# Kernel optimization log

Measured on AMD Instinct MI355X. Metric: run time of the kernel, lower is better.

The kernel has to match this reference:

```python
import jax, jax.numpy as jnp
import numpy as np
from jax import lax

V = 100000       # vocab_size / num_words
E = 300          # embedding_size (== num_units, required by compare stage)
M = 300          # num_units / mem_dim
NC = 3           # num_classes
L = 128          # leaves per tree -> N = 2L-1 nodes
N = 2 * L - 1


def build_tree(num_leaves):
    # balanced binary tree, postorder node numbering (children before parent)
    left, right = [], []
    def rec(lo, hi):
        if hi - lo == 1:
            left.append(-1); right.append(-1)
            return len(left) - 1
        mid = (lo + hi) // 2
        l = rec(lo, mid)
        r = rec(mid, hi)
        left.append(l); right.append(r)
        return len(left) - 1
    rec(0, num_leaves)
    return np.asarray(left, np.int32), np.asarray(right, np.int32)


def setup_inputs() -> dict:
    key = jax.random.key(0)
    ks = jax.random.split(key, 20)
    l1, r1 = build_tree(L)
    l2, r2 = build_tree(L)
    s = 0.1  # param scale (stands in for orthogonal init)
    inp = {
        "sent1": jax.random.randint(ks[0], (N,), 0, V),
        "sent2": jax.random.randint(ks[1], (N,), 0, V),
        "left1": jnp.asarray(l1), "right1": jnp.asarray(r1),
        "left2": jnp.asarray(l2), "right2": jnp.asarray(r2),
        "emb": jax.random.normal(ks[2], (V, E), jnp.float32),
        # composer x-projections, gate order: [cx, ix, fx, ox]
        "Wx_i": jax.random.normal(ks[3], (4, M, E), jnp.float32) * s,
        "bx_i": jnp.zeros((4, M), jnp.float32),
        # composer h-projections, gate order: [u, i, lf, rf, o]
        "Wl_i": jax.random.normal(ks[4], (5, M, M), jnp.float32) * s,
        "Wr_i": jax.random.normal(ks[5], (5, M, M), jnp.float32) * s,
        "Wx_c": jax.random.normal(ks[6], (4, M, M), jnp.float32) * s,
        "bx_c": jnp.zeros((4, M), jnp.float32),
        "Wl_c": jax.random.normal(ks[7], (5, M, M), jnp.float32) * s,
        "Wr_c": jax.random.normal(ks[8], (5, M, M), jnp.float32) * s,
        "Wc": jax.random.normal(ks[9], (M, 4 * M), jnp.float32) * 0.01,
        "bc": jnp.zeros((M,), jnp.float32),
        "Wa1": jax.random.normal(ks[10], (M, 4 * M), jnp.float32) * 0.01,
        "ba1": jnp.zeros((M,), jnp.float32),
        "Wa2": jax.random.normal(ks[11], (NC, M), jnp.float32) * 0.01,
        "ba2": jnp.zeros((NC,), jnp.float32),
    }
    return inp


def tree_lstm(xg, left, right, Wl, Wr):
    # xg: [N, 4, M] precomputed x-gate terms (cx, ix, fx, ox)
    # Wl/Wr: [5, M, M] hidden-state gate weights (u, i, lf, rf, o)
    n, _, m = xg.shape
    zero = jnp.zeros((m,), xg.dtype)

    def step(carry, t):
        C, H = carry
        i, l, r = t
        lc = jnp.where(l >= 0, C[jnp.maximum(l, 0)], zero)
        lh = jnp.where(l >= 0, H[jnp.maximum(l, 0)], zero)
        rc = jnp.where(r >= 0, C[jnp.maximum(r, 0)], zero)
        rh = jnp.where(r >= 0, H[jnp.maximum(r, 0)], zero)
        gl = jnp.einsum('gmd,d->gm', Wl, lh)  # [5, M]
        gr = jnp.einsum('gmd,d->gm', Wr, rh)
        x = xg[i]  # [4, M]
        u  = jnp.tanh(x[0] + gl[0] + gr[0])
        ig = jax.nn.sigmoid(x[1] + gl[1] + gr[1])
        lf = jax.nn.sigmoid(x[2] + gl[2] + gr[2])  # fx shared for both forgets (as in source)
        rf = jax.nn.sigmoid(x[2] + gl[3] + gr[3])
        c = ig * u + lf * lc + rf * rc
        o = jax.nn.sigmoid(x[3] + gl[4] + gr[4])
        h = o * jnp.tanh(c)
        return (C.at[i].set(c), H.at[i].set(h)), None

    init = (jnp.zeros((n, m), xg.dtype), jnp.zeros((n, m), xg.dtype))
    (_, H), _ = lax.scan(step, init, (jnp.arange(n), left, right))
    return H  # [N, M] all node hidden states in postorder


def reference(sent1, sent2, left1, right1, left2, right2, emb,
              Wx_i, bx_i, Wl_i, Wr_i, Wx_c, bx_c, Wl_c, Wr_c,
              Wc, bc, Wa1, ba1, Wa2, ba2):
    pad = emb.shape[0] - 1  # num_words - 1

    def encode(sent, left, right):
        # leaves embed their token; internal nodes embed PAD (PAD=True path)
        tok = jnp.where(left < 0, sent, pad)
        x = emb[tok]                                        # [N, E]
        xg = jnp.einsum('nd,gmd->ngm', x, Wx_i) + bx_i      # [N, 4, M]
        return tree_lstm(xg, left, right, Wl_i, Wr_i)

    s1 = encode(sent1, left1, right1)  # [N1, M]
    s2 = encode(sent2, left2, right2)  # [N2, M]

    raw = s1 @ s2.T                                         # [N1, N2]
    beta = jax.nn.softmax(raw, axis=1) @ s2                 # aligned to s1
    alpha = jax.nn.softmax(raw.T, axis=1) @ s1              # aligned to s2

    def compare(s, a, left, right):
        feat = jnp.concatenate([s, a, s - a, s * a], axis=-1)  # [N, 4M]
        h = jax.nn.relu(feat @ Wc.T + bc)                      # [N, M]
        xg = jnp.einsum('nd,gmd->ngm', h, Wx_c) + bx_c
        return tree_lstm(xg, left, right, Wl_c, Wr_c)

    v1 = compare(s1, beta, left1, right1)
    v2 = compare(s2, alpha, left2, right2)

    agg = jnp.concatenate([v1.mean(0), v1.max(0), v2.mean(0), v2.max(0)])  # [4M]
    hidden = jax.nn.relu(agg @ Wa1.T + ba1)
    logits = hidden @ Wa2.T + ba2
    return logits[None, :]  # [1, num_classes]
```

## Files before the change

### kernel.cpp

```cpp
#include <hip/hip_runtime.h>
#include <math.h>

#define NN 255
#define MM 300
#define TC 510
#define NBLK 300
#define CHUNK 16
#define HTLD 512

__device__ __forceinline__ float sigm(float x) { return 1.0f / (1.0f + expf(-x)); }

__device__ __forceinline__ float aload(const float* p) {
  return __hip_atomic_load(p, __ATOMIC_RELAXED, __HIP_MEMORY_SCOPE_AGENT);
}
__device__ __forceinline__ void astore(float* p, float v) {
  __hip_atomic_store(p, v, __ATOMIC_RELAXED, __HIP_MEMORY_SCOPE_AGENT);
}

__device__ __forceinline__ void leaf_gate(const float* __restrict__ xgp, int m, float& c, float& h) {
  float x0 = xgp[m], x1 = xgp[300 + m], x3 = xgp[900 + m];
  float u  = tanhf(x0);
  float ig = sigm(x1);
  c = ig * u;
  h = sigm(x3) * tanhf(c);
}

__device__ __forceinline__ void gsync(unsigned* flags, unsigned phase) {
  asm volatile("s_waitcnt vmcnt(0)" ::: "memory");
  __syncthreads();
  unsigned* gate = flags + NBLK;
  if (blockIdx.x == 0) {
    if (threadIdx.x < 64) {
      for (;;) {
        unsigned mn = phase;
        for (int i = 1 + (int)threadIdx.x; i < NBLK; i += 64)
          mn = min(mn, __hip_atomic_load(&flags[i], __ATOMIC_RELAXED, __HIP_MEMORY_SCOPE_AGENT));
        if (__all(mn >= phase)) break;
        __builtin_amdgcn_s_sleep(2);
      }
      if (threadIdx.x == 0)
        __hip_atomic_store(gate, phase, __ATOMIC_RELAXED, __HIP_MEMORY_SCOPE_AGENT);
    }
  } else {
    if (threadIdx.x == 0) {
      __hip_atomic_store(&flags[blockIdx.x], phase, __ATOMIC_RELAXED, __HIP_MEMORY_SCOPE_AGENT);
      while (__hip_atomic_load(gate, __ATOMIC_RELAXED, __HIP_MEMORY_SCOPE_AGENT) < phase)
        __builtin_amdgcn_s_sleep(2);
    }
  }
  __syncthreads();
}

__global__ __launch_bounds__(512) void k_setup(const int* __restrict__ l1, const int* __restrict__ r1,
                                               const int* __restrict__ l2, const int* __restrict__ r2,
                                               int4* __restrict__ lists2, int* __restrict__ cnt)
{
  __shared__ int lv[TC];
  __shared__ int cs[16];
  int t = threadIdx.x;
  if (t < TC) lv[t] = 0;
  if (t < 16) cs[t] = 0;
  __syncthreads();
  for (int it = 0; it < 12; ++it) {
    int nv = 0;
    if (t < TC) {
      int tr = t >= NN;
      int i  = t - tr * NN;
      const int* L = tr ? l2 : l1;
      const int* R = tr ? r2 : r1;
      int l = L[i], r = R[i];
      nv = (l < 0) ? 0 : 1 + max(lv[tr * NN + l], lv[tr * NN + r]);
    }
    __syncthreads();
    if (t < TC) lv[t] = nv;
    __syncthreads();
  }
  if (t < TC) {
    int tr = t >= NN;
    int i  = t - tr * NN;
    int v  = min(lv[t], 15);
    int pos = atomicAdd(&cs[v], 1);
    int l = (tr ? l2 : l1)[i], r = (tr ? r2 : r1)[i];
    lists2[v * 256 + pos] = make_int4(tr * NN + i, tr * NN + max(l, 0), tr * NN + max(r, 0), 0);
  }
  __syncthreads();
  if (t < 16) cnt[t] = cs[t];
}

__global__ __launch_bounds__(256, 2) void k_tree(
    const int* __restrict__ l1, const int* __restrict__ l2,
    const float* __restrict__ Wl, const float* __restrict__ Wr,
    const float* __restrict__ xg,
    float* __restrict__ H, float* __restrict__ C, float* __restrict__ HT,
    const int4* __restrict__ lists2, const int* __restrict__ cnt,
    unsigned* __restrict__ bar)
{
  __shared__ float Hs[CHUNK][2][320];
  __shared__ float Cs[CHUNK][4][2];
  __shared__ float Xs[CHUNK][4][4];
  __shared__ int4 nfo[288];
  __shared__ int lvoff[9];

  const int tid  = threadIdx.x;
  const int lane = tid & 63;
  const int team = tid >> 6;
  const int mblk = blockIdx.x % 75;
  const int grp  = blockIdx.x / 75;
  const int m    = mblk * 4 + team;

  float wl[5][5], wr[5][5];
  #pragma unroll
  for (int g = 0; g < 5; ++g) {
    #pragma unroll
    for (int j = 0; j < 5; ++j) {
      int d = j * 64 + lane;
      size_t o = ((size_t)g * 300 + m) * 300 + d;
      wl[g][j] = (d < 300) ? Wl[o] : 0.f;
      wr[g][j] = (d < 300) ? Wr[o] : 0.f;
    }
  }

  if (tid == 0) { int o = 0; for (int lv = 1; lv <= 7; ++lv) { lvoff[lv] = o; o += cnt[lv]; } }
  __syncthreads();
  for (int lv = 1; lv <= 7; ++lv)
    for (int i = tid; i < cnt[lv]; i += 256)
      nfo[lvoff[lv] + i] = lists2[lv * 256 + i];

  for (int e = blockIdx.x * 256 + tid; e < TC * 300; e += 256 * NBLK) {
    int gi = e / 300;
    int mm = e - gi * 300;
    int tr = gi >= NN;
    int node = gi - tr * NN;
    if ((tr ? l2 : l1)[node] < 0) {
      float c, h;
      leaf_gate(xg + (size_t)gi * 1200, mm, c, h);
      astore(&C[(size_t)gi * 300 + mm], c);
      astore(&H[(size_t)gi * 300 + mm], h);
      astore(&HT[(size_t)mm * HTLD + gi], h);
    }
  }
  gsync(bar, 1);

  for (int lv = 1; lv <= 7; ++lv) {
    int nodes = cnt[lv];
    int npg = (nodes + 3) >> 2;
    int n0 = grp * npg;
    int n1 = min(nodes, n0 + npg);
    for (int nb = n0; nb < n1; nb += CHUNK) {
      int nch = min(CHUNK, n1 - nb);
      int base = lvoff[lv] + nb;
      __syncthreads();

      #pragma unroll
      for (int p = 0; p < 2; ++p) {
        int niA = team + p * 8;
        int niB = niA + 4;
        bool vA = niA < nch, vB = niB < nch;
        int4 na = vA ? nfo[base + niA] : make_int4(0, 0, 0, 0);
        int4 nb4 = vB ? nfo[base + niB] : make_int4(0, 0, 0, 0);
        float bA0, bA1, bA2, bA3, bA4, bA5, bA6, bA7, bA8, bA9;
        float bB0, bB1, bB2, bB3, bB4, bB5, bB6, bB7, bB8, bB9;
        #define LD(side_ptr, d, ok) ((ok) ? aload(&H[(size_t)(side_ptr) * 300 + (d)]) : 0.f)
        {
          int d0 = lane, d1 = 64 + lane, d2 = 128 + lane, d3 = 192 + lane, d4 = 256 + lane;
          bool i4 = d4 < 300;
          bA0 = LD(na.y, d0, vA); bA1 = LD(na.y, d1, vA); bA2 = LD(na.y, d2, vA);
          bA3 = LD(na.y, d3, vA); bA4 = LD(na.y, d4, vA && i4);
          bA5 = LD(na.z, d0, vA); bA6 = LD(na.z, d1, vA); bA7 = LD(na.z, d2, vA);
          bA8 = LD(na.z, d3, vA); bA9 = LD(na.z, d4, vA && i4);
          bB0 = LD(nb4.y, d0, vB); bB1 = LD(nb4.y, d1, vB); bB2 = LD(nb4.y, d2, vB);
          bB3 = LD(nb4.y, d3, vB); bB4 = LD(nb4.y, d4, vB && i4);
          bB5 = LD(nb4.z, d0, vB); bB6 = LD(nb4.z, d1, vB); bB7 = LD(nb4.z, d2, vB);
          bB8 = LD(nb4.z, d3, vB); bB9 = LD(nb4.z, d4, vB && i4);
          if (vA) {
            Hs[niA][0][d0] = bA0; Hs[niA][0][d1] = bA1; Hs[niA][0][d2] = bA2;
            Hs[niA][0][d3] = bA3; Hs[niA][0][d4] = bA4;
            Hs[niA][1][d0] = bA5; Hs[niA][1][d1] = bA6; Hs[niA][1][d2] = bA7;
            Hs[niA][1][d3] = bA8; Hs[niA][1][d4] = bA9;
          }
          if (vB) {
            Hs[niB][0][d0] = bB0; Hs[niB][0][d1] = bB1; Hs[niB][0][d2] = bB2;
            Hs[niB][0][d3] = bB3; Hs[niB][0][d4] = bB4;
            Hs[niB][1][d0] = bB5; Hs[niB][1][d1] = bB6; Hs[niB][1][d2] = bB7;
            Hs[niB][1][d3] = bB8; Hs[niB][1][d4] = bB9;
          }
        }
        #undef LD
      }
      if (tid < 128) {
        int ni = tid >> 3, tm = (tid >> 1) & 3, side = tid & 1;
        if (ni < nch) {
          int4 nn = nfo[base + ni];
          int child = side ? nn.z : nn.y;
          Cs[ni][tm][side] = aload(&C[(size_t)child * 300 + mblk * 4 + tm]);
        }
      }
      {
        int ni = tid >> 4, tm = (tid >> 2) & 3, g = tid & 3;
        if (ni < nch) {
          int4 nn = nfo[base + ni];
          Xs[ni][tm][g] = xg[(size_t)nn.x * 1200 + g * 300 + mblk * 4 + tm];
        }
      }
      __syncthreads();

      #pragma unroll 2
      for (int ni = 0; ni < nch; ++ni) {
        float p0 = 0.f, p1 = 0.f, p2 = 0.f, p3 = 0.f, p4 = 0.f;
        #pragma unroll
        for (int j = 0; j < 5; ++j) {
          float hl = Hs[ni][0][j * 64 + lane];
          float hr = Hs[ni][1][j * 64 + lane];
          p0 += wl[0][j] * hl + wr[0][j] * hr;
          p1 += wl[1][j] * hl + wr[1][j] * hr;
          p2 += wl[2][j] * hl + wr[2][j] * hr;
          p3 += wl[3][j] * hl + wr[3][j] * hr;
          p4 += wl[4][j] * hl + wr[4][j] * hr;
        }
        #pragma unroll
        for (int off = 32; off; off >>= 1) {
          p0 += __shfl_xor(p0, off);
          p1 += __shfl_xor(p1, off);
          p2 += __shfl_xor(p2, off);
          p3 += __shfl_xor(p3, off);
          p4 += __shfl_xor(p4, off);
        }
        if (lane == 0) {
          int4 nn = nfo[base + ni];
          int gi = nn.x;
          float lc = Cs[ni][team][0], rc = Cs[ni][team][1];
          float u  = tanhf(Xs[ni][team][0] + p0);
          float ig = sigm (Xs[ni][team][1] + p1);
          float lf = sigm (Xs[ni][team][2] + p2);
          float rf = sigm (Xs[ni][team][2] + p3);
          float o  = sigm (Xs[ni][team][3] + p4);
          float cc = ig * u + lf * lc + rf * rc;
          float hv = o * tanhf(cc);
          astore(&C[(size_t)gi * 300 + m], cc);
          astore(&H[(size_t)gi * 300 + m], hv);
          astore(&HT[(size_t)m * HTLD + gi], hv);
        }
      }
    }
    if (lv < 7) gsync(bar, 1 + lv);
  }
}

__global__ __launch_bounds__(256) void k_xg(const int* __restrict__ sent1, const int* __restrict__ sent2,
                                            const int* __restrict__ l1, const int* __restrict__ l2,
                                            const float* __restrict__ emb, int pad,
                                            const float* __restrict__ W, const float* __restrict__ bias,
                                            const float* __restrict__ hsrc, float* __restrict__ out)
{
  __shared__ float Z[8][300];
  int tx = threadIdx.x, ty = threadIdx.y;
  int t = ty * 64 + tx;
  int colbase = blockIdx.y * 8;
  for (int c = 0; c < 8; ++c) {
    int gcol = colbase + c;
    if (gcol < TC) {
      if (hsrc) {
        for (int k = t; k < 300; k += 256) Z[c][k] = hsrc[(size_t)gcol * 300 + k];
      } else {
        int tr = gcol >= NN;
        int node = gcol - tr * NN;
        const int* L = tr ? l2 : l1;
        const int* S = tr ? sent2 : sent1;
        int tok = (L[node] < 0) ? S[node] : pad;
        const float* e = emb + (size_t)tok * 300;
        for (int k = t; k < 300; k += 256) Z[c][k] = e[k];
      }
    } else {
      for (int k = t; k < 300; k += 256) Z[c][k] = 0.f;
    }
  }
  __syncthreads();
  int r = blockIdx.x * 64 + tx;
  if (r < 1200) {
    float a0 = 0.f, a1 = 0.f;
    const float* wp = W + (size_t)r * 300;
    for (int k = 0; k < 300; k += 4) {
      float4 wv = *(const float4*)(wp + k);
      float4 z0 = *(const float4*)(&Z[ty][k]);
      float4 z1 = *(const float4*)(&Z[ty + 4][k]);
      a0 += wv.x*z0.x + wv.y*z0.y + wv.z*z0.z + wv.w*z0.w;
      a1 += wv.x*z1.x + wv.y*z1.y + wv.z*z1.z + wv.w*z1.w;
    }
    float b = bias[r];
    int g0 = colbase + ty, g1 = colbase + ty + 4;
    if (g0 < TC) out[(size_t)g0 * 1200 + r] = a0 + b;
    if (g1 < TC) out[(size_t)g1 * 1200 + r] = a1 + b;
  }
}

__global__ __launch_bounds__(256) void k_attn(const float* __restrict__ H, const float* __restrict__ HT,
                                              float* __restrict__ ab)
{
  __shared__ float q[300];
  __shared__ float pr[NN];
  __shared__ float red[256];
  int b = blockIdx.x, t = threadIdx.x;
  int dir = b >= NN;
  int i = b - dir * NN;
  const float* Ss = H + (dir ? NN * 300 : 0);
  const float* So = H + (dir ? 0 : NN * 300);
  int oppb = dir ? 0 : NN;
  for (int k = t; k < 300; k += 256) q[k] = Ss[(size_t)i * 300 + k];
  __syncthreads();
  float v = -1e30f;
  if (t < NN) {
    float a = 0.f;
    const float* hp = HT + oppb + t;
    #pragma unroll 4
    for (int k = 0; k < 300; ++k) a += q[k] * hp[(size_t)k * HTLD];
    pr[t] = a;
    v = a;
  }
  red[t] = v;
  __syncthreads();
  for (int s = 128; s > 0; s >>= 1) { if (t < s) red[t] = fmaxf(red[t], red[t + s]); __syncthreads(); }
  float mx = red[0];
  __syncthreads();
  float e = 0.f;
  if (t < NN) { e = expf(pr[t] - mx); pr[t] = e; }
  red[t] = e;
  __syncthreads();
  for (int s = 128; s > 0; s >>= 1) { if (t < s) red[t] += red[t + s]; __syncthreads(); }
  float inv = 1.0f / red[0];
  __syncthreads();
  for (int m = t; m < 300; m += 256) {
    float a = 0.f;
    for (int j = 0; j < NN; ++j) a += pr[j] * So[(size_t)j * 300 + m];
    ab[(size_t)b * 300 + m] = a * inv;
  }
}

__global__ __launch_bounds__(256) void k_hcmp(const float* __restrict__ Henc, const float* __restrict__ ab,
                                              const float* __restrict__ Wc, const float* __restrict__ bc,
                                              float* __restrict__ hc)
{
  __shared__ float Z[8][1200];
  int tx = threadIdx.x, ty = threadIdx.y;
  int t = ty * 64 + tx;
  int colbase = blockIdx.y * 8;
  for (int c = 0; c < 8; ++c) {
    int gcol = colbase + c;
    if (gcol < TC) {
      const float* sp = Henc + (size_t)gcol * 300;
      const float* ap = ab + (size_t)gcol * 300;
      for (int k = t; k < 1200; k += 256) {
        int sel = k >= 900 ? 3 : (k >= 600 ? 2 : (k >= 300 ? 1 : 0));
        int kk = k - sel * 300;
        float s = sp[kk], a = ap[kk];
        Z[c][k] = sel == 0 ? s : sel == 1 ? a : sel == 2 ? (s - a) : (s * a);
      }
    } else {
      for (int k = t; k < 1200; k += 256) Z[c][k] = 0.f;
    }
  }
  __syncthreads();
  int r = blockIdx.x * 64 + tx;
  if (r < 300) {
    float a0 = 0.f, a1 = 0.f;
    const float* wp = Wc + (size_t)r * 1200;
    for (int k = 0; k < 1200; k += 4) {
      float4 wv = *(const float4*)(wp + k);
      float4 z0 = *(const float4*)(&Z[ty][k]);
      float4 z1 = *(const float4*)(&Z[ty + 4][k]);
      a0 += wv.x*z0.x + wv.y*z0.y + wv.z*z0.z + wv.w*z0.w;
      a1 += wv.x*z1.x + wv.y*z1.y + wv.z*z1.z + wv.w*z1.w;
    }
    float b = bc[r];
    int g0 = colbase + ty, g1 = colbase + ty + 4;
    if (g0 < TC) hc[(size_t)g0 * 300 + r] = fmaxf(a0 + b, 0.f);
    if (g1 < TC) hc[(size_t)g1 * 300 + r] = fmaxf(a1 + b, 0.f);
  }
}

__global__ __launch_bounds__(512) void k_head(const float* __restrict__ HTc,
                                              const float* __restrict__ Wa1, const float* __restrict__ ba1,
                                              const float* __restrict__ Wa2, const float* __restrict__ ba2,
                                              float* __restrict__ out)
{
  __shared__ float a_s[1200];
  __shared__ float hid[300];
  int t = threadIdx.x;
  for (int idx = t; idx < 600; idx += 512) {
    int tr = idx >= 300;
    int m = idx - tr * 300;
    const float* p = HTc + (size_t)m * HTLD + tr * NN;
    float s = 0.f, mx = -1e30f;
    for (int n = 0; n < NN; ++n) { float v = p[n]; s += v; mx = fmaxf(mx, v); }
    a_s[tr * 600 + m] = s / 255.0f;
    a_s[tr * 600 + 300 + m] = mx;
  }
  __syncthreads();
  for (int h = t; h < 300; h += 512) {
    float acc = ba1[h];
    const float* wp = Wa1 + (size_t)h * 1200;
    for (int k = 0; k < 1200; k += 4) {
      float4 wv = *(const float4*)(wp + k);
      float4 av = *(const float4*)(&a_s[k]);
      acc += wv.x*av.x + wv.y*av.y + wv.z*av.z + wv.w*av.w;
    }
    hid[h] = fmaxf(acc, 0.f);
  }
  __syncthreads();
  if (t < 192) {
    int c = t >> 6, lane = t & 63;
    float a = 0.f;
    for (int k = lane; k < 300; k += 64) a += Wa2[c * 300 + k] * hid[k];
    for (int off = 32; off > 0; off >>= 1) a += __shfl_down(a, off);
    if (lane == 0) out[c] = a + ba2[c];
  }
}

extern "C" void kernel_launch(void* const* d_in, const int* in_sizes, int n_in,
                              void* d_out, int out_size, void* d_ws, size_t ws_size,
                              hipStream_t stream)
{
  const int*   sent1 = (const int*)d_in[0];
  const int*   sent2 = (const int*)d_in[1];
  const int*   l1    = (const int*)d_in[2];
  const int*   r1    = (const int*)d_in[3];
  const int*   l2    = (const int*)d_in[4];
  const int*   r2    = (const int*)d_in[5];
  const float* emb   = (const float*)d_in[6];
  const float* Wx_i  = (const float*)d_in[7];
  const float* bx_i  = (const float*)d_in[8];
  const float* Wl_i  = (const float*)d_in[9];
  const float* Wr_i  = (const float*)d_in[10];
  const float* Wx_c  = (const float*)d_in[11];
  const float* bx_c  = (const float*)d_in[12];
  const float* Wl_c  = (const float*)d_in[13];
  const float* Wr_c  = (const float*)d_in[14];
  const float* Wc    = (const float*)d_in[15];
  const float* bc    = (const float*)d_in[16];
  const float* Wa1   = (const float*)d_in[17];
  const float* ba1   = (const float*)d_in[18];
  const float* Wa2   = (const float*)d_in[19];
  const float* ba2   = (const float*)d_in[20];
  int V = in_sizes[6] / 300;
  int pad = V - 1;

  char* w = (char*)d_ws;
  unsigned* bar1 = (unsigned*)w;
  unsigned* bar2 = (unsigned*)(w + 2048);
  int* cnt     = (int*)(w + 4096);
  int4* lists2 = (int4*)(w + 4160);
  float* xg   = (float*)(w + 4160 + 65536);
  float* Henc = xg + 612000;
  float* Hcmp = Henc + 153000;
  float* C    = Hcmp + 153000;
  float* ab   = C + 153000;
  float* hc   = ab + 153000;
  float* HTe  = hc + 153000;
  float* HTc  = HTe + 153600;

  hipMemsetAsync((void*)bar1, 0, 4096, stream);
  k_setup<<<1, 512, 0, stream>>>(l1, r1, l2, r2, lists2, cnt);

  dim3 blk(64, 4);

  k_xg<<<dim3(19, 64), blk, 0, stream>>>(sent1, sent2, l1, l2, emb, pad, Wx_i, bx_i, nullptr, xg);
  {
    void* args[] = {(void*)&l1, (void*)&l2,
                    (void*)&Wl_i, (void*)&Wr_i, (void*)&xg,
                    (void*)&Henc, (void*)&C, (void*)&HTe,
                    (void*)&lists2, (void*)&cnt, (void*)&bar1};
    hipLaunchCooperativeKernel((void*)k_tree, dim3(NBLK), dim3(256), args, 0, stream);
  }

  k_attn<<<TC, 256, 0, stream>>>(Henc, HTe, ab);

  k_hcmp<<<dim3(5, 64), blk, 0, stream>>>(Henc, ab, Wc, bc, hc);
  k_xg<<<dim3(19, 64), blk, 0, stream>>>(sent1, sent2, l1, l2, emb, pad, Wx_c, bx_c, hc, xg);
  {
    void* args[] = {(void*)&l1, (void*)&l2,
                    (void*)&Wl_c, (void*)&Wr_c, (void*)&xg,
                    (void*)&Hcmp, (void*)&C, (void*)&HTc,
                    (void*)&lists2, (void*)&cnt, (void*)&bar2};
    hipLaunchCooperativeKernel((void*)k_tree, dim3(NBLK), dim3(256), args, 0, stream);
  }

  k_head<<<1, 512, 0, stream>>>(HTc, Wa1, ba1, Wa2, ba2, (float*)d_out);
}
```

Baseline: 503.8 us.

## Fuse whole pipeline into one persistent cooperative kernel with grid barriers

Merges setup, x-projections, both tree-LSTM stages, attention, compare MLP, aggregation and head into a single cooperative kernel of 600 blocks, separated by software grid barriers. The goal is to remove the multiple kernel launches and the gaps between them. Tree levels are now split across 8 node groups instead of 4, with smaller chunks and packed 32-bit child lists. The cost is many more grid-wide barriers with 600 participating blocks, and a fallback to the old multi-kernel path when the occupancy check fails.

```diff
diff --git a/kernel.cpp b/kernel.cpp
--- a/kernel.cpp
+++ b/kernel.cpp
@@ -2,54 +2,433 @@
 #include <math.h>
 
 #define NN 255
-#define MM 300
 #define TC 510
-#define NBLK 300
-#define CHUNK 16
 #define HTLD 512
-
-__device__ __forceinline__ float sigm(float x) { return 1.0f / (1.0f + expf(-x)); }
-
-__device__ __forceinline__ float aload(const float* p) {
-  return __hip_atomic_load(p, __ATOMIC_RELAXED, __HIP_MEMORY_SCOPE_AGENT);
-}
-__device__ __forceinline__ void astore(float* p, float v) {
-  __hip_atomic_store(p, v, __ATOMIC_RELAXED, __HIP_MEMORY_SCOPE_AGENT);
-}
-
-__device__ __forceinline__ void leaf_gate(const float* __restrict__ xgp, int m, float& c, float& h) {
-  float x0 = xgp[m], x1 = xgp[300 + m], x3 = xgp[900 + m];
-  float u  = tanhf(x0);
-  float ig = sigm(x1);
+#define FNB 600
+#define FNG 8
+#define FCH 12
+#define BNB 300
+#define BCH 16
+
+typedef unsigned int uint32;
+
+__device__ __forceinline__ float sigm(float x){ return 1.f/(1.f+expf(-x)); }
+
+__device__ __forceinline__ float aload(const float* p){ return __hip_atomic_load(p, __ATOMIC_RELAXED, __HIP_MEMORY_SCOPE_AGENT); }
+__device__ __forceinline__ void astore(float* p, float v){ __hip_atomic_store(p, v, __ATOMIC_RELAXED, __HIP_MEMORY_SCOPE_AGENT); }
+__device__ __forceinline__ uint32 aloadu(const uint32* p){ return __hip_atomic_load(p, __ATOMIC_RELAXED, __HIP_MEMORY_SCOPE_AGENT); }
+__device__ __forceinline__ void astoreu(uint32* p, uint32 v){ __hip_atomic_store(p, v, __ATOMIC_RELAXED, __HIP_MEMORY_SCOPE_AGENT); }
+
+__device__ __forceinline__ void leaf_gate(const float* __restrict__ xgp, int m, float& c, float& h){
+  float x0 = xgp[m], x1 = xgp[300+m], x3 = xgp[900+m];
+  float u = tanhf(x0), ig = sigm(x1);
   c = ig * u;
   h = sigm(x3) * tanhf(c);
 }
 
-__device__ __forceinline__ void gsync(unsigned* flags, unsigned phase) {
+template<int NB>
+__device__ __forceinline__ void gsync(uint32* flags, uint32 phase){
   asm volatile("s_waitcnt vmcnt(0)" ::: "memory");
   __syncthreads();
-  unsigned* gate = flags + NBLK;
-  if (blockIdx.x == 0) {
-    if (threadIdx.x < 64) {
-      for (;;) {
-        unsigned mn = phase;
-        for (int i = 1 + (int)threadIdx.x; i < NBLK; i += 64)
-          mn = min(mn, __hip_atomic_load(&flags[i], __ATOMIC_RELAXED, __HIP_MEMORY_SCOPE_AGENT));
+  uint32* gate = flags + NB;
+  if (blockIdx.x == 0){
+    if (threadIdx.x < 64){
+      for(;;){
+        uint32 mn = phase;
+        for (int i = 1 + (int)threadIdx.x; i < NB; i += 64)
+          mn = min(mn, aloadu(&flags[i]));
         if (__all(mn >= phase)) break;
         __builtin_amdgcn_s_sleep(2);
       }
-      if (threadIdx.x == 0)
-        __hip_atomic_store(gate, phase, __ATOMIC_RELAXED, __HIP_MEMORY_SCOPE_AGENT);
+      if (threadIdx.x == 0) astoreu(gate, phase);
     }
   } else {
-    if (threadIdx.x == 0) {
-      __hip_atomic_store(&flags[blockIdx.x], phase, __ATOMIC_RELAXED, __HIP_MEMORY_SCOPE_AGENT);
-      while (__hip_atomic_load(gate, __ATOMIC_RELAXED, __HIP_MEMORY_SCOPE_AGENT) < phase)
-        __builtin_amdgcn_s_sleep(2);
-    }
-  }
-  __syncthreads();
-}
+    if (threadIdx.x == 0){
+      astoreu(&flags[blockIdx.x], phase);
+      while (aloadu(gate) < phase) __builtin_amdgcn_s_sleep(2);
+    }
+  }
+  __syncthreads();
+}
+
+__global__ __launch_bounds__(256, 4) void k_all(
+  const int* __restrict__ sent1, const int* __restrict__ sent2,
+  const int* __restrict__ l1, const int* __restrict__ r1,
+  const int* __restrict__ l2, const int* __restrict__ r2,
+  const float* __restrict__ emb, int pad,
+  const float* __restrict__ Wx_i, const float* __restrict__ bx_i,
+  const float* __restrict__ Wl_i, const float* __restrict__ Wr_i,
+  const float* __restrict__ Wx_c, const float* __restrict__ bx_c,
+  const float* __restrict__ Wl_c, const float* __restrict__ Wr_c,
+  const float* __restrict__ Wcm, const float* __restrict__ bcm,
+  const float* __restrict__ Wa1, const float* __restrict__ ba1,
+  const float* __restrict__ Wa2, const float* __restrict__ ba2,
+  float* __restrict__ out,
+  float* __restrict__ xg_e, float* __restrict__ xg_c,
+  float* __restrict__ H, float* __restrict__ C,
+  float* __restrict__ ab, float* __restrict__ hc,
+  float* __restrict__ HT, float* __restrict__ agg,
+  uint32* __restrict__ lists, uint32* __restrict__ cntg,
+  uint32* __restrict__ bar)
+{
+  __shared__ float ubuf[7680];
+  __shared__ float Cs[FCH][4][2];
+  __shared__ float Xs[FCH][4][4];
+  __shared__ uint32 nfo_s[256];
+  __shared__ int lvoff_s[9];
+  __shared__ int cnt_s[16];
+  __shared__ float red_s[256];
+
+  const int b = blockIdx.x, tid = threadIdx.x;
+  const int lane = tid & 63, team = tid >> 6;
+  const int mblk = b % 75, grp = b / 75;
+  const int m = mblk * 4 + team;
+  int ph = 0;
+
+  auto xg_tiles = [&](const float* W, const float* bias, const float* hsrc,
+                      float* outp, int t0, int stride){
+    float (*Z)[300] = (float(*)[300])ubuf;
+    for (int t = t0; t < 1216; t += stride){
+      int rb = t % 19, cb = t / 19;
+      int colbase = cb * 8;
+      __syncthreads();
+      for (int k = tid; k < 2400; k += 256){
+        int c = k / 300, d = k - c * 300;
+        int gcol = colbase + c;
+        float v = 0.f;
+        if (gcol < TC){
+          if (hsrc) v = hsrc[(size_t)gcol * 300 + d];
+          else {
+            int tr = gcol >= NN, node = gcol - tr * NN;
+            int tok = ((tr ? l2 : l1)[node] < 0) ? (tr ? sent2 : sent1)[node] : pad;
+            v = emb[(size_t)tok * 300 + d];
+          }
+        }
+        Z[c][d] = v;
+      }
+      __syncthreads();
+      int r = rb * 64 + lane;
+      if (r < 1200){
+        float a0 = 0.f, a1 = 0.f;
+        const float* wp = W + (size_t)r * 300;
+        for (int k = 0; k < 300; k += 4){
+          float4 wv = *(const float4*)(wp + k);
+          float4 z0 = *(const float4*)(&Z[team][k]);
+          float4 z1 = *(const float4*)(&Z[team + 4][k]);
+          a0 += wv.x*z0.x + wv.y*z0.y + wv.z*z0.z + wv.w*z0.w;
+          a1 += wv.x*z1.x + wv.y*z1.y + wv.z*z1.z + wv.w*z1.w;
+        }
+        float bb = bias[r];
+        int g0 = colbase + team, g1 = g0 + 4;
+        if (g0 < TC) astore(&outp[(size_t)g0 * 1200 + r], a0 + bb);
+        if (g1 < TC) astore(&outp[(size_t)g1 * 1200 + r], a1 + bb);
+      }
+    }
+  };
+
+  if (b == 0){
+    int* lv = (int*)ubuf;
+    for (int i = tid; i < TC; i += 256) lv[i] = 0;
+    if (tid < 16) cnt_s[tid] = 0;
+    __syncthreads();
+    for (int it = 0; it < 12; ++it){
+      int nv0 = 0, nv1 = 0;
+      {
+        int i = tid;
+        int tr = i >= NN, node = i - tr * NN;
+        int l = (tr ? l2 : l1)[node], r = (tr ? r2 : r1)[node];
+        if (l >= 0) nv0 = 1 + max(lv[tr * NN + l], lv[tr * NN + r]);
+      }
+      {
+        int i = tid + 256;
+        if (i < TC){
+          int tr = i >= NN, node = i - tr * NN;
+          int l = (tr ? l2 : l1)[node], r = (tr ? r2 : r1)[node];
+          if (l >= 0) nv1 = 1 + max(lv[tr * NN + l], lv[tr * NN + r]);
+        }
+      }
+      __syncthreads();
+      lv[tid] = nv0;
+      if (tid + 256 < TC) lv[tid + 256] = nv1;
+      __syncthreads();
+    }
+    for (int i = tid; i < TC; i += 256){
+      int tr = i >= NN, node = i - tr * NN;
+      int v = min(lv[i], 15);
+      int pos = atomicAdd(&cnt_s[v], 1);
+      int l = (tr ? l2 : l1)[node], r = (tr ? r2 : r1)[node];
+      uint32 pk = (uint32)i | ((uint32)(tr * NN + max(l, 0)) << 10) | ((uint32)(tr * NN + max(r, 0)) << 20);
+      astoreu(&lists[v * 256 + pos], pk);
+    }
+    __syncthreads();
+    if (tid < 16) astoreu(&cntg[tid], (uint32)cnt_s[tid]);
+  } else {
+    xg_tiles(Wx_i, bx_i, nullptr, xg_e, b - 1, FNB - 1);
+  }
+  gsync<FNB>(bar, (uint32)++ph);
+
+  if (tid < 16) cnt_s[tid] = (int)aloadu(&cntg[tid]);
+  __syncthreads();
+  if (tid == 0){
+    lvoff_s[1] = 0;
+    for (int lv = 2; lv <= 7; ++lv) lvoff_s[lv] = lvoff_s[lv - 1] + cnt_s[lv - 1];
+  }
+  __syncthreads();
+  for (int lv = 1; lv <= 7; ++lv)
+    for (int i = tid; i < cnt_s[lv]; i += 256)
+      nfo_s[lvoff_s[lv] + i] = aloadu(&lists[lv * 256 + i]);
+  __syncthreads();
+
+  auto tree_stage = [&](const float* Wl, const float* Wr, const float* xgp){
+    float wl[5][5], wr[5][5];
+    #pragma unroll
+    for (int g = 0; g < 5; ++g)
+      #pragma unroll
+      for (int j = 0; j < 5; ++j){
+        int d = j * 64 + lane;
+        size_t o = ((size_t)g * 300 + m) * 300 + d;
+        wl[g][j] = (d < 300) ? Wl[o] : 0.f;
+        wr[g][j] = (d < 300) ? Wr[o] : 0.f;
+      }
+    for (int e = b * 256 + tid; e < TC * 300; e += 256 * FNB){
+      int gi = e / 300, mm = e - gi * 300;
+      int tr = gi >= NN, node = gi - tr * NN;
+      if (((tr ? l2 : l1)[node]) < 0){
+        float c, h; leaf_gate(xgp + (size_t)gi * 1200, mm, c, h);
+        astore(&C[(size_t)gi * 300 + mm], c);
+        astore(&H[(size_t)gi * 300 + mm], h);
+        astore(&HT[(size_t)mm * HTLD + gi], h);
+      }
+    }
+    gsync<FNB>(bar, (uint32)++ph);
+
+    float (*Hs)[2][320] = (float(*)[2][320])ubuf;
+    for (int lv = 1; lv <= 7; ++lv){
+      int nodes = cnt_s[lv];
+      int npg = (nodes + FNG - 1) / FNG;
+      int n0 = grp * npg, n1 = min(nodes, n0 + npg);
+      for (int nb0 = n0; nb0 < n1; nb0 += FCH){
+        int nch = min(FCH, n1 - nb0);
+        int base = lvoff_s[lv] + nb0;
+        __syncthreads();
+        #pragma unroll
+        for (int p = 0; p < 2; ++p){
+          int niA = team + p * 8, niB = niA + 4;
+          bool vA = niA < nch, vB = niB < nch;
+          uint32 na = vA ? nfo_s[base + niA] : 0u;
+          uint32 nk = vB ? nfo_s[base + niB] : 0u;
+          int aL = (na >> 10) & 1023, aR = (na >> 20) & 1023;
+          int bL = (nk >> 10) & 1023, bR = (nk >> 20) & 1023;
+          int d0 = lane, d1 = 64 + lane, d2 = 128 + lane, d3 = 192 + lane, d4 = 256 + lane;
+          bool i4 = d4 < 300;
+          #define LDH(ci, dd, ok) ((ok) ? aload(&H[(size_t)(ci) * 300 + (dd)]) : 0.f)
+          float a0=LDH(aL,d0,vA), a1=LDH(aL,d1,vA), a2=LDH(aL,d2,vA), a3=LDH(aL,d3,vA), a4=LDH(aL,d4,vA&&i4);
+          float a5=LDH(aR,d0,vA), a6=LDH(aR,d1,vA), a7=LDH(aR,d2,vA), a8=LDH(aR,d3,vA), a9=LDH(aR,d4,vA&&i4);
+          float c0=LDH(bL,d0,vB), c1=LDH(bL,d1,vB), c2=LDH(bL,d2,vB), c3=LDH(bL,d3,vB), c4=LDH(bL,d4,vB&&i4);
+          float c5=LDH(bR,d0,vB), c6=LDH(bR,d1,vB), c7=LDH(bR,d2,vB), c8=LDH(bR,d3,vB), c9=LDH(bR,d4,vB&&i4);
+          #undef LDH
+          if (vA){
+            Hs[niA][0][d0]=a0; Hs[niA][0][d1]=a1; Hs[niA][0][d2]=a2; Hs[niA][0][d3]=a3; Hs[niA][0][d4]=a4;
+            Hs[niA][1][d0]=a5; Hs[niA][1][d1]=a6; Hs[niA][1][d2]=a7; Hs[niA][1][d3]=a8; Hs[niA][1][d4]=a9;
+          }
+          if (vB){
+            Hs[niB][0][d0]=c0; Hs[niB][0][d1]=c1; Hs[niB][0][d2]=c2; Hs[niB][0][d3]=c3; Hs[niB][0][d4]=c4;
+            Hs[niB][1][d0]=c5; Hs[niB][1][d1]=c6; Hs[niB][1][d2]=c7; Hs[niB][1][d3]=c8; Hs[niB][1][d4]=c9;
+          }
+        }
+        if (tid < 128){
+          int ni = tid >> 3, tm = (tid >> 1) & 3, side = tid & 1;
+          if (ni < nch){
+            uint32 nn = nfo_s[base + ni];
+            int child = side ? ((nn >> 20) & 1023) : ((nn >> 10) & 1023);
+            Cs[ni][tm][side] = aload(&C[(size_t)child * 300 + mblk * 4 + tm]);
+          }
+        }
+        {
+          int ni = tid >> 4, tm = (tid >> 2) & 3, g = tid & 3;
+          if (ni < nch){
+            uint32 nn = nfo_s[base + ni];
+            int gi = nn & 1023;
+            Xs[ni][tm][g] = xgp[(size_t)gi * 1200 + g * 300 + mblk * 4 + tm];
+          }
+        }
+        __syncthreads();
+        #pragma unroll 2
+        for (int ni = 0; ni < nch; ++ni){
+          float p0 = 0.f, p1 = 0.f, p2 = 0.f, p3 = 0.f, p4 = 0.f;
+          #pragma unroll
+          for (int j = 0; j < 5; ++j){
+            float hl = Hs[ni][0][j * 64 + lane];
+            float hr = Hs[ni][1][j * 64 + lane];
+            p0 += wl[0][j] * hl + wr[0][j] * hr;
+            p1 += wl[1][j] * hl + wr[1][j] * hr;
+            p2 += wl[2][j] * hl + wr[2][j] * hr;
+            p3 += wl[3][j] * hl + wr[3][j] * hr;
+            p4 += wl[4][j] * hl + wr[4][j] * hr;
+          }
+          #pragma unroll
+          for (int off = 32; off; off >>= 1){
+            p0 += __shfl_xor(p0, off); p1 += __shfl_xor(p1, off); p2 += __shfl_xor(p2, off);
+            p3 += __shfl_xor(p3, off); p4 += __shfl_xor(p4, off);
+          }
+          if (lane == 0){
+            uint32 nn = nfo_s[base + ni];
+            int gi = nn & 1023;
+            float lc = Cs[ni][team][0], rc = Cs[ni][team][1];
+            float u  = tanhf(Xs[ni][team][0] + p0);
+            float ig = sigm (Xs[ni][team][1] + p1);
+            float lf = sigm (Xs[ni][team][2] + p2);
+            float rf = sigm (Xs[ni][team][2] + p3);
+            float o  = sigm (Xs[ni][team][3] + p4);
+            float cc = ig * u + lf * lc + rf * rc;
+            float hv = o * tanhf(cc);
+            astore(&C[(size_t)gi * 300 + m], cc);
+            astore(&H[(size_t)gi * 300 + m], hv);
+            astore(&HT[(size_t)m * HTLD + gi], hv);
+          }
+        }
+      }
+      gsync<FNB>(bar, (uint32)++ph);
+    }
+  };
+
+  tree_stage(Wl_i, Wr_i, xg_e);
+
+  {
+    float* q = ubuf;
+    float* pr = ubuf + 304;
+    for (int row = b; row < TC; row += FNB){
+      __syncthreads();
+      int dir = row >= NN, i = row - dir * NN;
+      const float* Ss = H + (dir ? (size_t)NN * 300 : (size_t)0);
+      const float* So = H + (dir ? (size_t)0 : (size_t)NN * 300);
+      int oppb = dir ? 0 : NN;
+      for (int k = tid; k < 300; k += 256) q[k] = Ss[(size_t)i * 300 + k];
+      __syncthreads();
+      float v = -1e30f;
+      if (tid < NN){
+        const float* hp = HT + oppb + tid;
+        float a = 0.f;
+        #pragma unroll 4
+        for (int k = 0; k < 300; ++k) a += q[k] * hp[(size_t)k * HTLD];
+        pr[tid] = a; v = a;
+      }
+      red_s[tid] = v; __syncthreads();
+      for (int s = 128; s; s >>= 1){ if (tid < s) red_s[tid] = fmaxf(red_s[tid], red_s[tid + s]); __syncthreads(); }
+      float mx = red_s[0]; __syncthreads();
+      float e = 0.f;
+      if (tid < NN){ e = expf(pr[tid] - mx); pr[tid] = e; }
+      red_s[tid] = e; __syncthreads();
+      for (int s = 128; s; s >>= 1){ if (tid < s) red_s[tid] += red_s[tid + s]; __syncthreads(); }
+      float inv = 1.f / red_s[0]; __syncthreads();
+      for (int mm = tid; mm < 300; mm += 256){
+        float a = 0.f;
+        for (int j = 0; j < NN; ++j) a += pr[j] * So[(size_t)j * 300 + mm];
+        astore(&ab[(size_t)row * 300 + mm], a * inv);
+      }
+    }
+  }
+  gsync<FNB>(bar, (uint32)++ph);
+
+  {
+    float (*Z)[1200] = (float(*)[1200])ubuf;
+    for (int t = b; t < 425; t += FNB){
+      int rb = t % 5, cb = t / 5;
+      int colbase = cb * 6;
+      __syncthreads();
+      for (int k = tid; k < 7200; k += 256){
+        int c = k / 1200, rem = k - c * 1200;
+        int gcol = colbase + c;
+        float v = 0.f;
+        if (gcol < TC){
+          int sel = rem >= 900 ? 3 : rem >= 600 ? 2 : rem >= 300 ? 1 : 0;
+          int kk = rem - sel * 300;
+          float s = H[(size_t)gcol * 300 + kk], a = ab[(size_t)gcol * 300 + kk];
+          v = sel == 0 ? s : sel == 1 ? a : sel == 2 ? (s - a) : (s * a);
+        }
+        Z[c][rem] = v;
+      }
+      __syncthreads();
+      int r = rb * 64 + lane;
+      if (r < 300){
+        int c0 = team, c1 = team + 4;
+        bool v1 = c1 < 6;
+        float a0 = 0.f, a1 = 0.f;
+        const float* wp = Wcm + (size_t)r * 1200;
+        for (int k = 0; k < 1200; k += 4){
+          float4 wv = *(const float4*)(wp + k);
+          float4 z0 = *(const float4*)(&Z[c0][k]);
+          a0 += wv.x*z0.x + wv.y*z0.y + wv.z*z0.z + wv.w*z0.w;
+          if (v1){
+            float4 z1 = *(const float4*)(&Z[c1][k]);
+            a1 += wv.x*z1.x + wv.y*z1.y + wv.z*z1.z + wv.w*z1.w;
+          }
+        }
+        float bb = bcm[r];
+        int g0 = colbase + c0;
+        if (g0 < TC) astore(&hc[(size_t)g0 * 300 + r], fmaxf(a0 + bb, 0.f));
+        if (v1){
+          int g1 = colbase + c1;
+          if (g1 < TC) astore(&hc[(size_t)g1 * 300 + r], fmaxf(a1 + bb, 0.f));
+        }
+      }
+    }
+  }
+  gsync<FNB>(bar, (uint32)++ph);
+
+  xg_tiles(Wx_c, bx_c, hc, xg_c, b, FNB);
+  gsync<FNB>(bar, (uint32)++ph);
+
+  tree_stage(Wl_c, Wr_c, xg_c);
+
+  {
+    for (int idx = b; idx < 600; idx += FNB){
+      int tr = idx / 300, mm = idx - tr * 300;
+      const float* p = HT + (size_t)mm * HTLD + tr * NN;
+      float v = 0.f, vm = -1e30f;
+      if (tid < NN){ v = aload(&p[tid]); vm = v; }
+      __syncthreads();
+      red_s[tid] = v; __syncthreads();
+      for (int s = 128; s; s >>= 1){ if (tid < s) red_s[tid] += red_s[tid + s]; __syncthreads(); }
+      float sum = red_s[0]; __syncthreads();
+      red_s[tid] = vm; __syncthreads();
+      for (int s = 128; s; s >>= 1){ if (tid < s) red_s[tid] = fmaxf(red_s[tid], red_s[tid + s]); __syncthreads(); }
+      if (tid == 0){
+        astore(&agg[tr * 600 + mm], sum / 255.f);
+        astore(&agg[tr * 600 + 300 + mm], red_s[0]);
+      }
+      __syncthreads();
+    }
+  }
+  gsync<FNB>(bar, (uint32)++ph);
+
+  if (b == 0){
+    float* a_s = ubuf;
+    float* hid = ubuf + 1200;
+    for (int k = tid; k < 1200; k += 256) a_s[k] = aload(&agg[k]);
+    __syncthreads();
+    for (int h = tid; h < 300; h += 256){
+      float acc = ba1[h];
+      const float* wp = Wa1 + (size_t)h * 1200;
+      for (int k = 0; k < 1200; k += 4){
+        float4 wv = *(const float4*)(wp + k);
+        float4 av = *(const float4*)(&a_s[k]);
+        acc += wv.x*av.x + wv.y*av.y + wv.z*av.z + wv.w*av.w;
+      }
+      hid[h] = fmaxf(acc, 0.f);
+    }
+    __syncthreads();
+    if (tid < 192){
+      int c = tid >> 6, ln = tid & 63;
+      float a = 0.f;
+      for (int k = ln; k < 300; k += 64) a += Wa2[c * 300 + k] * hid[k];
+      #pragma unroll
+      for (int off = 32; off; off >>= 1) a += __shfl_down(a, off);
+      if (ln == 0) out[c] = a + ba2[c];
+    }
+  }
+}
+
 
 __global__ __launch_bounds__(512) void k_setup(const int* __restrict__ l1, const int* __restrict__ r1,
                                                const int* __restrict__ l2, const int* __restrict__ r2,
@@ -61,11 +440,10 @@
   if (t < TC) lv[t] = 0;
   if (t < 16) cs[t] = 0;
   __syncthreads();
-  for (int it = 0; it < 12; ++it) {
+  for (int it = 0; it < 12; ++it){
     int nv = 0;
-    if (t < TC) {
-      int tr = t >= NN;
-      int i  = t - tr * NN;
+    if (t < TC){
+      int tr = t >= NN, i = t - tr * NN;
       const int* L = tr ? l2 : l1;
       const int* R = tr ? r2 : r1;
       int l = L[i], r = R[i];
@@ -75,10 +453,9 @@
     if (t < TC) lv[t] = nv;
     __syncthreads();
   }
-  if (t < TC) {
-    int tr = t >= NN;
-    int i  = t - tr * NN;
-    int v  = min(lv[t], 15);
+  if (t < TC){
+    int tr = t >= NN, i = t - tr * NN;
+    int v = min(lv[t], 15);
     int pos = atomicAdd(&cs[v], 1);
     int l = (tr ? l2 : l1)[i], r = (tr ? r2 : r1)[i];
     lists2[v * 256 + pos] = make_int4(tr * NN + i, tr * NN + max(l, 0), tr * NN + max(r, 0), 0);
@@ -93,103 +470,82 @@
     const float* __restrict__ xg,
     float* __restrict__ H, float* __restrict__ C, float* __restrict__ HT,
     const int4* __restrict__ lists2, const int* __restrict__ cnt,
-    unsigned* __restrict__ bar)
+    uint32* __restrict__ bar)
 {
-  __shared__ float Hs[CHUNK][2][320];
-  __shared__ float Cs[CHUNK][4][2];
-  __shared__ float Xs[CHUNK][4][4];
+  __shared__ float Hs[BCH][2][320];
+  __shared__ float Cs[BCH][4][2];
+  __shared__ float Xs[BCH][4][4];
   __shared__ int4 nfo[288];
   __shared__ int lvoff[9];
 
-  const int tid  = threadIdx.x;
-  const int lane = tid & 63;
-  const int team = tid >> 6;
-  const int mblk = blockIdx.x % 75;
-  const int grp  = blockIdx.x / 75;
-  const int m    = mblk * 4 + team;
+  const int tid = threadIdx.x;
+  const int lane = tid & 63, team = tid >> 6;
+  const int mblk = blockIdx.x % 75, grp = blockIdx.x / 75;
+  const int m = mblk * 4 + team;
 
   float wl[5][5], wr[5][5];
   #pragma unroll
-  for (int g = 0; g < 5; ++g) {
+  for (int g = 0; g < 5; ++g)
     #pragma unroll
-    for (int j = 0; j < 5; ++j) {
+    for (int j = 0; j < 5; ++j){
       int d = j * 64 + lane;
       size_t o = ((size_t)g * 300 + m) * 300 + d;
       wl[g][j] = (d < 300) ? Wl[o] : 0.f;
       wr[g][j] = (d < 300) ? Wr[o] : 0.f;
     }
-  }
-
-  if (tid == 0) { int o = 0; for (int lv = 1; lv <= 7; ++lv) { lvoff[lv] = o; o += cnt[lv]; } }
+
+  if (tid == 0){ int o = 0; for (int lv = 1; lv <= 7; ++lv){ lvoff[lv] = o; o += cnt[lv]; } }
   __syncthreads();
   for (int lv = 1; lv <= 7; ++lv)
     for (int i = tid; i < cnt[lv]; i += 256)
       nfo[lvoff[lv] + i] = lists2[lv * 256 + i];
 
-  for (int e = blockIdx.x * 256 + tid; e < TC * 300; e += 256 * NBLK) {
-    int gi = e / 300;
-    int mm = e - gi * 300;
-    int tr = gi >= NN;
-    int node = gi - tr * NN;
-    if ((tr ? l2 : l1)[node] < 0) {
-      float c, h;
-      leaf_gate(xg + (size_t)gi * 1200, mm, c, h);
+  for (int e = blockIdx.x * 256 + tid; e < TC * 300; e += 256 * BNB){
+    int gi = e / 300, mm = e - gi * 300;
+    int tr = gi >= NN, node = gi - tr * NN;
+    if ((tr ? l2 : l1)[node] < 0){
+      float c, h; leaf_gate(xg + (size_t)gi * 1200, mm, c, h);
       astore(&C[(size_t)gi * 300 + mm], c);
       astore(&H[(size_t)gi * 300 + mm], h);
       astore(&HT[(size_t)mm * HTLD + gi], h);
     }
   }
-  gsync(bar, 1);
-
-  for (int lv = 1; lv <= 7; ++lv) {
+  gsync<BNB>(bar, 1);
+
+  for (int lv = 1; lv <= 7; ++lv){
     int nodes = cnt[lv];
     int npg = (nodes + 3) >> 2;
-    int n0 = grp * npg;
-    int n1 = min(nodes, n0 + npg);
-    for (int nb = n0; nb < n1; nb += CHUNK) {
-      int nch = min(CHUNK, n1 - nb);
-      int base = lvoff[lv] + nb;
-      __syncthreads();
-
+    int n0 = grp * npg, n1 = min(nodes, n0 + npg);
+    for (int nb0 = n0; nb0 < n1; nb0 += BCH){
+      int nch = min(BCH, n1 - nb0);
+      int base = lvoff[lv] + nb0;
+      __syncthreads();
       #pragma unroll
-      for (int p = 0; p < 2; ++p) {
-        int niA = team + p * 8;
-        int niB = niA + 4;
+      for (int p = 0; p < 2; ++p){
+        int niA = team + p * 8, niB = niA + 4;
         bool vA = niA < nch, vB = niB < nch;
         int4 na = vA ? nfo[base + niA] : make_int4(0, 0, 0, 0);
         int4 nb4 = vB ? nfo[base + niB] : make_int4(0, 0, 0, 0);
-        float bA0, bA1, bA2, bA3, bA4, bA5, bA6, bA7, bA8, bA9;
-        float bB0, bB1, bB2, bB3, bB4, bB5, bB6, bB7, bB8, bB9;
-        #define LD(side_ptr, d, ok) ((ok) ? aload(&H[(size_t)(side_ptr) * 300 + (d)]) : 0.f)
-        {
-          int d0 = lane, d1 = 64 + lane, d2 = 128 + lane, d3 = 192 + lane, d4 = 256 + lane;
-          bool i4 = d4 < 300;
-          bA0 = LD(na.y, d0, vA); bA1 = LD(na.y, d1, vA); bA2 = LD(na.y, d2, vA);
-          bA3 = LD(na.y, d3, vA); bA4 = LD(na.y, d4, vA && i4);
-          bA5 = LD(na.z, d0, vA); bA6 = LD(na.z, d1, vA); bA7 = LD(na.z, d2, vA);
-          bA8 = LD(na.z, d3, vA); bA9 = LD(na.z, d4, vA && i4);
-          bB0 = LD(nb4.y, d0, vB); bB1 = LD(nb4.y, d1, vB); bB2 = LD(nb4.y, d2, vB);
-          bB3 = LD(nb4.y, d3, vB); bB4 = LD(nb4.y, d4, vB && i4);
-          bB5 = LD(nb4.z, d0, vB); bB6 = LD(nb4.z, d1, vB); bB7 = LD(nb4.z, d2, vB);
-          bB8 = LD(nb4.z, d3, vB); bB9 = LD(nb4.z, d4, vB && i4);
-          if (vA) {
-            Hs[niA][0][d0] = bA0; Hs[niA][0][d1] = bA1; Hs[niA][0][d2] = bA2;
-            Hs[niA][0][d3] = bA3; Hs[niA][0][d4] = bA4;
-            Hs[niA][1][d0] = bA5; Hs[niA][1][d1] = bA6; Hs[niA][1][d2] = bA7;
-            Hs[niA][1][d3] = bA8; Hs[niA][1][d4] = bA9;
-          }
-          if (vB) {
-            Hs[niB][0][d0] = bB0; Hs[niB][0][d1] = bB1; Hs[niB][0][d2] = bB2;
-            Hs[niB][0][d3] = bB3; Hs[niB][0][d4] = bB4;
-            Hs[niB][1][d0] = bB5; Hs[niB][1][d1] = bB6; Hs[niB][1][d2] = bB7;
-            Hs[niB][1][d3] = bB8; Hs[niB][1][d4] = bB9;
-          }
-        }
-        #undef LD
-      }
-      if (tid < 128) {
+        int d0 = lane, d1 = 64 + lane, d2 = 128 + lane, d3 = 192 + lane, d4 = 256 + lane;
+        bool i4 = d4 < 300;
+        #define LDH(ci, dd, ok) ((ok) ? aload(&H[(size_t)(ci) * 300 + (dd)]) : 0.f)
+        float a0=LDH(na.y,d0,vA), a1=LDH(na.y,d1,vA), a2=LDH(na.y,d2,vA), a3=LDH(na.y,d3,vA), a4=LDH(na.y,d4,vA&&i4);
+        float a5=LDH(na.z,d0,vA), a6=LDH(na.z,d1,vA), a7=LDH(na.z,d2,vA), a8=LDH(na.z,d3,vA), a9=LDH(na.z,d4,vA&&i4);
+        float c0=LDH(nb4.y,d0,vB), c1=LDH(nb4.y,d1,vB), c2=LDH(nb4.y,d2,vB), c3=LDH(nb4.y,d3,vB), c4=LDH(nb4.y,d4,vB&&i4);
+        float c5=LDH(nb4.z,d0,vB), c6=LDH(nb4.z,d1,vB), c7=LDH(nb4.z,d2,vB), c8=LDH(nb4.z,d3,vB), c9=LDH(nb4.z,d4,vB&&i4);
+        #undef LDH
+        if (vA){
+          Hs[niA][0][d0]=a0; Hs[niA][0][d1]=a1; Hs[niA][0][d2]=a2; Hs[niA][0][d3]=a3; Hs[niA][0][d4]=a4;
+          Hs[niA][1][d0]=a5; Hs[niA][1][d1]=a6; Hs[niA][1][d2]=a7; Hs[niA][1][d3]=a8; Hs[niA][1][d4]=a9;
+        }
+        if (vB){
+          Hs[niB][0][d0]=c0; Hs[niB][0][d1]=c1; Hs[niB][0][d2]=c2; Hs[niB][0][d3]=c3; Hs[niB][0][d4]=c4;
+          Hs[niB][1][d0]=c5; Hs[niB][1][d1]=c6; Hs[niB][1][d2]=c7; Hs[niB][1][d3]=c8; Hs[niB][1][d4]=c9;
+        }
+      }
+      if (tid < 128){
         int ni = tid >> 3, tm = (tid >> 1) & 3, side = tid & 1;
-        if (ni < nch) {
+        if (ni < nch){
           int4 nn = nfo[base + ni];
           int child = side ? nn.z : nn.y;
           Cs[ni][tm][side] = aload(&C[(size_t)child * 300 + mblk * 4 + tm]);
@@ -197,18 +553,17 @@
       }
       {
         int ni = tid >> 4, tm = (tid >> 2) & 3, g = tid & 3;
-        if (ni < nch) {
+        if (ni < nch){
           int4 nn = nfo[base + ni];
           Xs[ni][tm][g] = xg[(size_t)nn.x * 1200 + g * 300 + mblk * 4 + tm];
         }
       }
       __syncthreads();
-
       #pragma unroll 2
-      for (int ni = 0; ni < nch; ++ni) {
+      for (int ni = 0; ni < nch; ++ni){
         float p0 = 0.f, p1 = 0.f, p2 = 0.f, p3 = 0.f, p4 = 0.f;
         #pragma unroll
-        for (int j = 0; j < 5; ++j) {
+        for (int j = 0; j < 5; ++j){
           float hl = Hs[ni][0][j * 64 + lane];
           float hr = Hs[ni][1][j * 64 + lane];
           p0 += wl[0][j] * hl + wr[0][j] * hr;
@@ -218,14 +573,11 @@
           p4 += wl[4][j] * hl + wr[4][j] * hr;
         }
         #pragma unroll
-        for (int off = 32; off; off >>= 1) {
-          p0 += __shfl_xor(p0, off);
-          p1 += __shfl_xor(p1, off);
-          p2 += __shfl_xor(p2, off);
-          p3 += __shfl_xor(p3, off);
-          p4 += __shfl_xor(p4, off);
-        }
-        if (lane == 0) {
+        for (int off = 32; off; off >>= 1){
+          p0 += __shfl_xor(p0, off); p1 += __shfl_xor(p1, off); p2 += __shfl_xor(p2, off);
+          p3 += __shfl_xor(p3, off); p4 += __shfl_xor(p4, off);
+        }
+        if (lane == 0){
           int4 nn = nfo[base + ni];
           int gi = nn.x;
           float lc = Cs[ni][team][0], rc = Cs[ni][team][1];
@@ -242,7 +594,7 @@
         }
       }
     }
-    if (lv < 7) gsync(bar, 1 + lv);
+    if (lv < 7) gsync<BNB>(bar, 1 + lv);
   }
 }
 
@@ -256,17 +608,14 @@
   int tx = threadIdx.x, ty = threadIdx.y;
   int t = ty * 64 + tx;
   int colbase = blockIdx.y * 8;
-  for (int c = 0; c < 8; ++c) {
+  for (int c = 0; c < 8; ++c){
     int gcol = colbase + c;
-    if (gcol < TC) {
-      if (hsrc) {
+    if (gcol < TC){
+      if (hsrc){
         for (int k = t; k < 300; k += 256) Z[c][k] = hsrc[(size_t)gcol * 300 + k];
       } else {
-        int tr = gcol >= NN;
-        int node = gcol - tr * NN;
-        const int* L = tr ? l2 : l1;
-        const int* S = tr ? sent2 : sent1;
-        int tok = (L[node] < 0) ? S[node] : pad;
+        int tr = gcol >= NN, node = gcol - tr * NN;
+        int tok = ((tr ? l2 : l1)[node] < 0) ? (tr ? sent2 : sent1)[node] : pad;
         const float* e = emb + (size_t)tok * 300;
         for (int k = t; k < 300; k += 256) Z[c][k] = e[k];
       }
@@ -276,10 +625,10 @@
   }
   __syncthreads();
   int r = blockIdx.x * 64 + tx;
-  if (r < 1200) {
+  if (r < 1200){
     float a0 = 0.f, a1 = 0.f;
     const float* wp = W + (size_t)r * 300;
-    for (int k = 0; k < 300; k += 4) {
+    for (int k = 0; k < 300; k += 4){
       float4 wv = *(const float4*)(wp + k);
       float4 z0 = *(const float4*)(&Z[ty][k]);
       float4 z1 = *(const float4*)(&Z[ty + 4][k]);
@@ -300,35 +649,29 @@
   __shared__ float pr[NN];
   __shared__ float red[256];
   int b = blockIdx.x, t = threadIdx.x;
-  int dir = b >= NN;
-  int i = b - dir * NN;
+  int dir = b >= NN, i = b - dir * NN;
   const float* Ss = H + (dir ? NN * 300 : 0);
   const float* So = H + (dir ? 0 : NN * 300);
   int oppb = dir ? 0 : NN;
   for (int k = t; k < 300; k += 256) q[k] = Ss[(size_t)i * 300 + k];
   __syncthreads();
   float v = -1e30f;
-  if (t < NN) {
+  if (t < NN){
     float a = 0.f;
     const float* hp = HT + oppb + t;
     #pragma unroll 4
     for (int k = 0; k < 300; ++k) a += q[k] * hp[(size_t)k * HTLD];
-    pr[t] = a;
-    v = a;
-  }
-  red[t] = v;
-  __syncthreads();
-  for (int s = 128; s > 0; s >>= 1) { if (t < s) red[t] = fmaxf(red[t], red[t + s]); __syncthreads(); }
-  float mx = red[0];
-  __syncthreads();
+    pr[t] = a; v = a;
+  }
+  red[t] = v; __syncthreads();
+  for (int s = 128; s; s >>= 1){ if (t < s) red[t] = fmaxf(red[t], red[t + s]); __syncthreads(); }
+  float mx = red[0]; __syncthreads();
   float e = 0.f;
-  if (t < NN) { e = expf(pr[t] - mx); pr[t] = e; }
-  red[t] = e;
-  __syncthreads();
-  for (int s = 128; s > 0; s >>= 1) { if (t < s) red[t] += red[t + s]; __syncthreads(); }
-  float inv = 1.0f / red[0];
-  __syncthreads();
-  for (int m = t; m < 300; m += 256) {
+  if (t < NN){ e = expf(pr[t] - mx); pr[t] = e; }
+  red[t] = e; __syncthreads();
+  for (int s = 128; s; s >>= 1){ if (t < s) red[t] += red[t + s]; __syncthreads(); }
+  float inv = 1.f / red[0]; __syncthreads();
+  for (int m = t; m < 300; m += 256){
     float a = 0.f;
     for (int j = 0; j < NN; ++j) a += pr[j] * So[(size_t)j * 300 + m];
     ab[(size_t)b * 300 + m] = a * inv;
@@ -343,12 +686,12 @@
   int tx = threadIdx.x, ty = threadIdx.y;
   int t = ty * 64 + tx;
   int colbase = blockIdx.y * 8;
-  for (int c = 0; c < 8; ++c) {
+  for (int c = 0; c < 8; ++c){
     int gcol = colbase + c;
-    if (gcol < TC) {
+    if (gcol < TC){
       const float* sp = Henc + (size_t)gcol * 300;
       const float* ap = ab + (size_t)gcol * 300;
-      for (int k = t; k < 1200; k += 256) {
+      for (int k = t; k < 1200; k += 256){
         int sel = k >= 900 ? 3 : (k >= 600 ? 2 : (k >= 300 ? 1 : 0));
         int kk = k - sel * 300;
         float s = sp[kk], a = ap[kk];
@@ -360,10 +703,10 @@
   }
   __syncthreads();
   int r = blockIdx.x * 64 + tx;
-  if (r < 300) {
+  if (r < 300){
     float a0 = 0.f, a1 = 0.f;
     const float* wp = Wc + (size_t)r * 1200;
-    for (int k = 0; k < 1200; k += 4) {
+    for (int k = 0; k < 1200; k += 4){
       float4 wv = *(const float4*)(wp + k);
       float4 z0 = *(const float4*)(&Z[ty][k]);
       float4 z1 = *(const float4*)(&Z[ty + 4][k]);
@@ -385,20 +728,20 @@
   __shared__ float a_s[1200];
   __shared__ float hid[300];
   int t = threadIdx.x;
-  for (int idx = t; idx < 600; idx += 512) {
+  for (int idx = t; idx < 600; idx += 512){
     int tr = idx >= 300;
     int m = idx - tr * 300;
     const float* p = HTc + (size_t)m * HTLD + tr * NN;
     float s = 0.f, mx = -1e30f;
-    for (int n = 0; n < NN; ++n) { float v = p[n]; s += v; mx = fmaxf(mx, v); }
+    for (int n = 0; n < NN; ++n){ float v = p[n]; s += v; mx = fmaxf(mx, v); }
     a_s[tr * 600 + m] = s / 255.0f;
     a_s[tr * 600 + 300 + m] = mx;
   }
   __syncthreads();
-  for (int h = t; h < 300; h += 512) {
+  for (int h = t; h < 300; h += 512){
     float acc = ba1[h];
     const float* wp = Wa1 + (size_t)h * 1200;
-    for (int k = 0; k < 1200; k += 4) {
+    for (int k = 0; k < 1200; k += 4){
       float4 wv = *(const float4*)(wp + k);
       float4 av = *(const float4*)(&a_s[k]);
       acc += wv.x*av.x + wv.y*av.y + wv.z*av.z + wv.w*av.w;
@@ -406,11 +749,11 @@
     hid[h] = fmaxf(acc, 0.f);
   }
   __syncthreads();
-  if (t < 192) {
+  if (t < 192){
     int c = t >> 6, lane = t & 63;
     float a = 0.f;
     for (int k = lane; k < 300; k += 64) a += Wa2[c * 300 + k] * hid[k];
-    for (int off = 32; off > 0; off >>= 1) a += __shfl_down(a, off);
+    for (int off = 32; off; off >>= 1) a += __shfl_down(a, off);
     if (lane == 0) out[c] = a + ba2[c];
   }
 }
@@ -434,8 +777,8 @@
   const float* bx_c  = (const float*)d_in[12];
   const float* Wl_c  = (const float*)d_in[13];
   const float* Wr_c  = (const float*)d_in[14];
-  const float* Wc    = (const float*)d_in[15];
-  const float* bc    = (const float*)d_in[16];
+  const float* Wcm   = (const float*)d_in[15];
+  const float* bcm   = (const float*)d_in[16];
   const float* Wa1   = (const float*)d_in[17];
   const float* ba1   = (const float*)d_in[18];
   const float* Wa2   = (const float*)d_in[19];
@@ -444,44 +787,61 @@
   int pad = V - 1;
 
   char* w = (char*)d_ws;
-  unsigned* bar1 = (unsigned*)w;
-  unsigned* bar2 = (unsigned*)(w + 2048);
-  int* cnt     = (int*)(w + 4096);
-  int4* lists2 = (int4*)(w + 4160);
-  float* xg   = (float*)(w + 4160 + 65536);
-  float* Henc = xg + 612000;
-  float* Hcmp = Henc + 153000;
-  float* C    = Hcmp + 153000;
+  uint32* bar    = (uint32*)w;
+  uint32* bar2   = (uint32*)(w + 2048);
+  int*    cnt    = (int*)(w + 8192);
+  uint32* listsP = (uint32*)(w + 8256);
+  int4*   lists2 = (int4*)(w + 24640);
+  float* fb   = (float*)(w + 90176);
+  float* xg_e = fb;
+  float* xg_c = xg_e + 612000;
+  float* H    = xg_c + 612000;
+  float* C    = H + 153000;
   float* ab   = C + 153000;
   float* hc   = ab + 153000;
-  float* HTe  = hc + 153000;
-  float* HTc  = HTe + 153600;
-
-  hipMemsetAsync((void*)bar1, 0, 4096, stream);
+  float* HT   = hc + 153000;
+  float* agg  = HT + 153600;
+  float* outp = (float*)d_out;
+
+  hipMemsetAsync(bar, 0, 4096, stream);
+
+  int nbF = 0, nCU = 0;
+  hipError_t eq = hipOccupancyMaxActiveBlocksPerMultiprocessor(&nbF, reinterpret_cast<const void*>(k_all), 256, 0);
+  hipError_t ec = hipDeviceGetAttribute(&nCU, hipDeviceAttributeMultiprocessorCount, 0);
+  bool fusedOK = (eq == hipSuccess) && (ec == hipSuccess) && (nbF * nCU >= FNB);
+
+  if (fusedOK){
+    void* args[] = { (void*)&sent1,(void*)&sent2,(void*)&l1,(void*)&r1,(void*)&l2,(void*)&r2,
+                     (void*)&emb,(void*)&pad,
+                     (void*)&Wx_i,(void*)&bx_i,(void*)&Wl_i,(void*)&Wr_i,
+                     (void*)&Wx_c,(void*)&bx_c,(void*)&Wl_c,(void*)&Wr_c,
+                     (void*)&Wcm,(void*)&bcm,(void*)&Wa1,(void*)&ba1,(void*)&Wa2,(void*)&ba2,
+                     (void*)&outp,
+                     (void*)&xg_e,(void*)&xg_c,(void*)&H,(void*)&C,(void*)&ab,(void*)&hc,
+                     (void*)&HT,(void*)&agg,(void*)&listsP,(void*)&cnt,(void*)&bar };
+    hipError_t el = hipLaunchCooperativeKernel((void*)k_all, dim3(FNB), dim3(256), args, 0, stream);
+    if (el == hipSuccess) return;
+    (void)hipGetLastError();
+  }
+
+  float* Hcmp = xg_c;
+  float* HTc  = xg_c + 153000;
+
   k_setup<<<1, 512, 0, stream>>>(l1, r1, l2, r2, lists2, cnt);
-
   dim3 blk(64, 4);
-
-  k_xg<<<dim3(19, 64), blk, 0, stream>>>(sent1, sent2, l1, l2, emb, pad, Wx_i, bx_i, nullptr, xg);
+  k_xg<<<dim3(19, 64), blk, 0, stream>>>(sent1, sent2, l1, l2, emb, pad, Wx_i, bx_i, nullptr, xg_e);
   {
-    void* args[] = {(void*)&l1, (void*)&l2,
-                    (void*)&Wl_i, (void*)&Wr_i, (void*)&xg,
-                    (void*)&Henc, (void*)&C, (void*)&HTe,
-                    (void*)&lists2, (void*)&cnt, (void*)&bar1};
-    hipLaunchCooperativeKernel((void*)k_tree, dim3(NBLK), dim3(256), args, 0, stream);
-  }
-
-  k_attn<<<TC, 256, 0, stream>>>(Henc, HTe, ab);
-
-  k_hcmp<<<dim3(5, 64), blk, 0, stream>>>(Henc, ab, Wc, bc, hc);
-  k_xg<<<dim3(19, 64), blk, 0, stream>>>(sent1, sent2, l1, l2, emb, pad, Wx_c, bx_c, hc, xg);
+    void* args[] = {(void*)&l1, (void*)&l2, (void*)&Wl_i, (void*)&Wr_i, (void*)&xg_e,
+                    (void*)&H, (void*)&C, (void*)&HT, (void*)&lists2, (void*)&cnt, (void*)&bar};
+    hipLaunchCooperativeKernel((void*)k_tree, dim3(BNB), dim3(256), args, 0, stream);
+  }
+  k_attn<<<TC, 256, 0, stream>>>(H, HT, ab);
+  k_hcmp<<<dim3(5, 64), blk, 0, stream>>>(H, ab, Wcm, bcm, hc);
+  k_xg<<<dim3(19, 64), blk, 0, stream>>>(sent1, sent2, l1, l2, emb, pad, Wx_c, bx_c, hc, xg_e);
   {
-    void* args[] = {(void*)&l1, (void*)&l2,
-                    (void*)&Wl_c, (void*)&Wr_c, (void*)&xg,
-                    (void*)&Hcmp, (void*)&C, (void*)&HTc,
-                    (void*)&lists2, (void*)&cnt, (void*)&bar2};
-    hipLaunchCooperativeKernel((void*)k_tree, dim3(NBLK), dim3(256), args, 0, stream);
-  }
-
-  k_head<<<1, 512, 0, stream>>>(HTc, Wa1, ba1, Wa2, ba2, (float*)d_out);
-}
+    void* args[] = {(void*)&l1, (void*)&l2, (void*)&Wl_c, (void*)&Wr_c, (void*)&xg_e,
+                    (void*)&Hcmp, (void*)&C, (void*)&HTc, (void*)&lists2, (void*)&cnt, (void*)&bar2};
+    hipLaunchCooperativeKernel((void*)k_tree, dim3(BNB), dim3(256), args, 0, stream);
+  }
+  k_head<<<1, 512, 0, stream>>>(HTc, Wa1, ba1, Wa2, ba2, outp);
+}
```

Result: no change. 496.0 us (-1.5%).
